# Performance work log

Hardware: AMD Instinct MI355X
Metric: run time of the kernel (lower is better)

## Reference

```python
import jax, jax.numpy as jnp
import numpy as np

B, Tu, Tm, Tz = 32, 128, 128, 32
V, H, E = 10000, 512, 128
S = E + H  # state_size


def setup_inputs() -> dict:
    key = jax.random.key(0)
    ks = jax.random.split(key, 24)
    u_input = jax.random.randint(ks[0], (B, Tu), 0, V)
    m_input = jax.random.randint(ks[1], (B, Tm), 0, V)
    pv_z_idx = jax.random.randint(ks[2], (B, Tz), 0, V)
    inp = {
        'u_input': u_input,
        'u_input_1hot': jax.nn.one_hot(u_input, V, dtype=jnp.float32),
        'u_hiddens': jax.random.normal(ks[3], (B, Tu, H), jnp.float32),
        'm_input': m_input,
        'm_input_1hot': jax.nn.one_hot(m_input, V, dtype=jnp.float32),
        'm_hiddens': jax.random.normal(ks[4], (B, Tm, H), jnp.float32),
        'pv_z_prob': jax.nn.softmax(jax.random.normal(ks[5], (B, Tz, V), jnp.float32), axis=-1),
        'pv_z_hidden': jax.random.normal(ks[6], (B, Tz, H), jnp.float32),
        'pv_z_idx': pv_z_idx,
        'emb_zt': jax.random.normal(ks[7], (B, 1, E), jnp.float32),
        'last_hidden': jax.random.normal(ks[8], (1, B, H), jnp.float32),
        # Attn params (concat attention: v . tanh(W [h; enc]))
        'W_attn': jax.random.normal(ks[9], (H, 2 * H), jnp.float32) * 0.02,
        'b_attn': jnp.zeros((H,), jnp.float32),
        'v_attn': jax.random.normal(ks[10], (H,), jnp.float32) * 0.05,
        # GRU params (torch gate order r,z,n)
        'W_ih': jax.random.normal(ks[11], (3 * H, S), jnp.float32) * 0.02,
        'W_hh': jax.random.normal(ks[12], (3 * H, H), jnp.float32) * 0.02,
        'b_ih': jnp.zeros((3 * H,), jnp.float32),
        'b_hh': jnp.zeros((3 * H,), jnp.float32),
        # generation / copy-score projections
        'W_gen': jax.random.normal(ks[13], (V, S), jnp.float32) * 0.02,
        'b_gen': jnp.zeros((V,), jnp.float32),
        'W_cpu': jax.random.normal(ks[14], (S, H), jnp.float32) * 0.02,
        'b_cpu': jnp.zeros((S,), jnp.float32),
        'W_cpm': jax.random.normal(ks[15], (S, H), jnp.float32) * 0.02,
        'b_cpm': jnp.zeros((S,), jnp.float32),
        'W_cppz': jax.random.normal(ks[16], (S, H), jnp.float32) * 0.02,
        'b_cppz': jnp.zeros((S,), jnp.float32),
    }
    return inp


def reference(u_input, u_input_1hot, u_hiddens, m_input, m_input_1hot, m_hiddens,
              pv_z_prob, pv_z_hidden, pv_z_idx, emb_zt, last_hidden,
              W_attn, b_attn, v_attn, W_ih, W_hh, b_ih, b_hh,
              W_gen, b_gen, W_cpu, b_cpu, W_cpm, b_cpm, W_cppz, b_cppz):
    Bv, Tuv, Vv = u_input_1hot.shape
    Tmv = m_hiddens.shape[1]
    t_input = emb_zt  # [B,1,E] (enable_selc_read=False)

    # ---- concat attention over [u; m; pv_z] hiddens ----
    enc = jnp.concatenate([u_hiddens, m_hiddens, pv_z_hidden], axis=1)  # [B,T,H]
    h0 = jnp.transpose(last_hidden, (1, 0, 2))  # [B,1,H]
    hid_rep = jnp.broadcast_to(h0, (Bv, enc.shape[1], h0.shape[2]))
    energy = jnp.tanh(jnp.einsum('bth,gh->btg', jnp.concatenate([hid_rep, enc], axis=2), W_attn) + b_attn)
    attn_w = jax.nn.softmax(jnp.einsum('bth,h->bt', energy, v_attn), axis=1)
    context = jnp.einsum('bt,bth->bh', attn_w, enc)[:, None, :]  # [B,1,H]

    # ---- single GRU step (torch gate order r,z,n) ----
    x = jnp.concatenate([t_input, context], axis=2)[:, 0, :]  # [B,E+H]
    h = h0[:, 0, :]
    gi = x @ W_ih.T + b_ih
    gh = h @ W_hh.T + b_hh
    i_r, i_z, i_n = jnp.split(gi, 3, axis=1)
    h_r, h_z, h_n = jnp.split(gh, 3, axis=1)
    r = jax.nn.sigmoid(i_r + h_r)
    z = jax.nn.sigmoid(i_z + h_z)
    n = jnp.tanh(i_n + r * h_n)
    h_new = (1.0 - z) * n + z * h  # [B,H]
    gru_out = h_new[:, None, :]
    last_hidden_new = h_new[None, :, :]

    # ---- generation + copy scores ----
    st = jnp.concatenate([h_new, t_input[:, 0, :]], axis=1)  # [B,E+H]
    score_g = st @ W_gen.T + b_gen  # [B,V]
    sc_u = jnp.einsum('bts,bs->bt', jnp.tanh(jnp.einsum('bth,sh->bts', u_hiddens, W_cpu) + b_cpu), st)
    sc_m = jnp.einsum('bts,bs->bt', jnp.tanh(jnp.einsum('bth,sh->bts', m_hiddens, W_cpm) + b_cpm), st)
    sc_pz = jnp.einsum('bts,bs->bt', jnp.tanh(jnp.einsum('bth,sh->bts', pv_z_hidden, W_cppz) + b_cppz), st)
    probs = jax.nn.softmax(jnp.concatenate([score_g, sc_u, sc_m, sc_pz], axis=1), axis=1)

    p_g = probs[:, :Vv]
    p_u = probs[:, Vv:Vv + Tuv]
    p_m = probs[:, Vv + Tuv:Vv + Tuv + Tmv]
    p_pz = probs[:, Vv + Tuv + Tmv:]
    prob_out = (p_g
                + jnp.einsum('bt,btv->bv', p_u, u_input_1hot)
                + jnp.einsum('bt,btv->bv', p_m, m_input_1hot)
                + jnp.einsum('bt,btv->bv', p_pz, pv_z_prob))
    return (prob_out, last_hidden_new, gru_out)
```

## Files before the change

### kernel.cpp

```cpp
#include <hip/hip_runtime.h>
#include <math.h>

#define B   32
#define TU  128
#define TM  128
#define TZ  32
#define TENC 288
#define V   10000
#define H   512
#define E   128
#define S   640
#define G3  1536
#define NLOG (V + TENC)

#define WS_Q      0
#define WS_SCORE  (WS_Q + B*H)
#define WS_CTX    (WS_SCORE + B*TENC)
#define WS_GI     (WS_CTX + B*H)
#define WS_GH     (WS_GI + B*G3)
#define WS_ST     (WS_GH + B*G3)
#define WS_LOGIT  (WS_ST + B*S)
#define WS_PCOPY  (WS_LOGIT + B*NLOG)
#define WS_F_TOTAL (WS_PCOPY + B*TENC)

#define BF_WA2  0
#define BF_WCP  (BF_WA2 + 512*512)
#define BF_ENC  (BF_WCP + 3*640*512)
#define BF_ST   (BF_ENC + B*TENC*H)
#define BF_TANH (BF_ST + B*S)

typedef __attribute__((ext_vector_type(8))) short bf16x8_t;
typedef __attribute__((ext_vector_type(4))) float f32x4_t;
typedef __attribute__((ext_vector_type(16))) float f32x16_t;

__device__ __forceinline__ float fast_tanh(float x) {
    return 1.f - 2.f / (__expf(2.f * x) + 1.f);
}

__device__ __forceinline__ unsigned short f2bf(float x) {
    unsigned int u = __float_as_uint(x);
    u += 0x7fffu + ((u >> 16) & 1u);
    return (unsigned short)(u >> 16);
}

__device__ __forceinline__ float bf2f(unsigned short u) {
    return __uint_as_float(((unsigned int)u) << 16);
}

__device__ __forceinline__ bf16x8_t cvt8(const float* p) {
    float4 a = *(const float4*)(p);
    float4 b = *(const float4*)(p + 4);
    bf16x8_t r;
    r[0] = (short)f2bf(a.x); r[1] = (short)f2bf(a.y);
    r[2] = (short)f2bf(a.z); r[3] = (short)f2bf(a.w);
    r[4] = (short)f2bf(b.x); r[5] = (short)f2bf(b.y);
    r[6] = (short)f2bf(b.z); r[7] = (short)f2bf(b.w);
    return r;
}

__device__ __forceinline__ const float* enc_row(const float* u, const float* m,
                                                const float* pz, int b, int t) {
    if (t < TU) return u + ((size_t)b * TU + t) * H;
    if (t < TU + TM) return m + ((size_t)b * TM + (t - TU)) * H;
    return pz + ((size_t)b * TZ + (t - TU - TM)) * H;
}

#define CVT_WA2_END  65536
#define CVT_TOTAL    (CVT_WA2_END + 3*81920)
#define CVTE_TOTAL   (B * TENC * 128)
#define CVT_ALL      (CVT_TOTAL + CVTE_TOTAL)
__global__ __launch_bounds__(256) void k_cvt_all(const float* __restrict__ W_attn,
                                                 const float* __restrict__ W_cpu,
                                                 const float* __restrict__ W_cpm,
                                                 const float* __restrict__ W_cppz,
                                                 const float* __restrict__ u_h,
                                                 const float* __restrict__ m_h,
                                                 const float* __restrict__ pz_h,
                                                 unsigned short* __restrict__ bf) {
    int idx = blockIdx.x * 256 + threadIdx.x;
    if (idx >= CVT_ALL) return;
    const float* src;
    unsigned short* dst;
    if (idx < CVT_WA2_END) {
        int g = idx >> 7, c4 = idx & 127;
        int k = c4 * 4, kt = k >> 5, kin = k & 31;
        src = W_attn + (size_t)g * 1024 + 512 + k;
        dst = bf + BF_WA2 + kt * (512 * 32) + g * 32 + kin;
    } else if (idx < CVT_TOTAL) {
        int r = idx - CVT_WA2_END;
        int seg = r / 81920, q = r % 81920;
        int s = q >> 7, c4 = q & 127;
        int k = c4 * 4, kt = k >> 5, kin = k & 31;
        const float* s0 = (seg == 0) ? W_cpu : (seg == 1) ? W_cpm : W_cppz;
        src = s0 + (size_t)s * 512 + k;
        dst = bf + BF_WCP + seg * 327680 + kt * (640 * 32) + s * 32 + kin;
    } else {
        int e = idx - CVT_TOTAL;
        int b = e / (TENC * 128);
        int r = e % (TENC * 128);
        int t = r >> 7, c4 = r & 127;
        int k = c4 * 4, kt = k >> 5, kin = k & 31;
        src = enc_row(u_h, m_h, pz_h, b, t) + k;
        dst = bf + BF_ENC + (((size_t)b * 16 + kt) * TENC + t) * 32 + kin;
    }
    float4 v = *(const float4*)src;
    ushort4 o;
    o.x = f2bf(v.x); o.y = f2bf(v.y); o.z = f2bf(v.z); o.w = f2bf(v.w);
    *(ushort4*)dst = o;
}

__global__ __launch_bounds__(64) void k_q_mfma(const float* __restrict__ last_h,
                                               const float* __restrict__ W_attn,
                                               const float* __restrict__ b_attn,
                                               float* __restrict__ ws) {
    int lane = threadIdx.x & 63;
    int m = lane & 31, khalf = lane >> 5;
    int n = blockIdx.x * 32 + m;
    const float* aptr = last_h + (size_t)m * H + khalf * 8;
    const float* bptr = W_attn + (size_t)n * 1024 + khalf * 8;
    f32x16_t acc = {};
    for (int k0 = 0; k0 < 512; k0 += 16) {
        bf16x8_t a = cvt8(aptr + k0);
        bf16x8_t bb = cvt8(bptr + k0);
        acc = __builtin_amdgcn_mfma_f32_32x32x16_bf16(a, bb, acc, 0, 0, 0);
    }
    float bg = b_attn[n];
#pragma unroll
    for (int r = 0; r < 16; ++r) {
        int row = (r & 3) + 8 * (r >> 2) + 4 * khalf;
        ws[WS_Q + row * H + n] = acc[r] + bg;
    }
}

__global__ __launch_bounds__(512) void k_enc_mfma(const unsigned short* __restrict__ bf,
                                                  const float* __restrict__ v_attn,
                                                  const float* __restrict__ b_cpu,
                                                  const float* __restrict__ b_cpm,
                                                  const float* __restrict__ b_cppz,
                                                  float* __restrict__ ws,
                                                  unsigned short* __restrict__ bft) {
    int blk = blockIdx.x;
    int b = blk / 9, t0 = (blk % 9) * 32;
    int tid = threadIdx.x, wave = tid >> 6, lane = tid & 63;
    int n16 = lane & 15, quad = lane >> 4;
    int seg = (t0 < TU) ? 0 : (t0 < TU + TM) ? 1 : 2;
    const float* bias = (seg == 0) ? b_cpu : (seg == 1) ? b_cpm : b_cppz;
    const unsigned short* abase =
        bf + BF_ENC + (((size_t)b * 16) * TENC + t0 + n16) * 32 + quad * 8;
    const unsigned short* wa =
        bf + BF_WA2 + (wave * 4) * (16 * 32) + n16 * 32 + quad * 8;
    const unsigned short* wc =
        bf + BF_WCP + seg * 327680 + (wave * 5) * (16 * 32) + n16 * 32 + quad * 8;
    f32x4_t accA[2][4], accC[2][5];
#pragma unroll
    for (int tl = 0; tl < 2; ++tl) {
#pragma unroll
        for (int j = 0; j < 4; ++j) accA[tl][j] = (f32x4_t){0.f, 0.f, 0.f, 0.f};
#pragma unroll
        for (int j = 0; j < 5; ++j) accC[tl][j] = (f32x4_t){0.f, 0.f, 0.f, 0.f};
    }
    for (int kt = 0; kt < 16; ++kt) {
        bf16x8_t a0 = *(const bf16x8_t*)(abase + (size_t)kt * TENC * 32);
        bf16x8_t a1 = *(const bf16x8_t*)(abase + (size_t)kt * TENC * 32 + 16 * 32);
        const unsigned short* wak = wa + (size_t)kt * 512 * 32;
        const unsigned short* wck = wc + (size_t)kt * 640 * 32;
#pragma unroll
        for (int j = 0; j < 4; ++j) {
            bf16x8_t bb = *(const bf16x8_t*)(wak + j * (16 * 32));
            accA[0][j] = __builtin_amdgcn_mfma_f32_16x16x32_bf16(a0, bb, accA[0][j], 0, 0, 0);
            accA[1][j] = __builtin_amdgcn_mfma_f32_16x16x32_bf16(a1, bb, accA[1][j], 0, 0, 0);
        }
#pragma unroll
        for (int j = 0; j < 5; ++j) {
            bf16x8_t bb = *(const bf16x8_t*)(wck + j * (16 * 32));
            accC[0][j] = __builtin_amdgcn_mfma_f32_16x16x32_bf16(a0, bb, accC[0][j], 0, 0, 0);
            accC[1][j] = __builtin_amdgcn_mfma_f32_16x16x32_bf16(a1, bb, accC[1][j], 0, 0, 0);
        }
    }
    float sval[2][4] = {{0.f, 0.f, 0.f, 0.f}, {0.f, 0.f, 0.f, 0.f}};
#pragma unroll
    for (int j = 0; j < 4; ++j) {
        int g = (wave * 4 + j) * 16 + n16;
        float q = ws[WS_Q + b * H + g];
        float va = v_attn[g];
#pragma unroll
        for (int tl = 0; tl < 2; ++tl)
#pragma unroll
            for (int r = 0; r < 4; ++r)
                sval[tl][r] += fast_tanh(accA[tl][j][r] + q) * va;
    }
#pragma unroll
    for (int tl = 0; tl < 2; ++tl)
#pragma unroll
        for (int r = 0; r < 4; ++r)
#pragma unroll
            for (int off = 8; off > 0; off >>= 1)
                sval[tl][r] += __shfl_down(sval[tl][r], off, 64);
    __shared__ float red[8][32];
    if (n16 == 0)
#pragma unroll
        for (int tl = 0; tl < 2; ++tl)
#pragma unroll
            for (int r = 0; r < 4; ++r)
                red[wave][tl * 16 + quad * 4 + r] = sval[tl][r];
#pragma unroll
    for (int j = 0; j < 5; ++j) {
        int s = (wave * 5 + j) * 16 + n16;
        float bi = bias[s];
#pragma unroll
        for (int tl = 0; tl < 2; ++tl)
#pragma unroll
            for (int r = 0; r < 4; ++r) {
                int t = t0 + tl * 16 + quad * 4 + r;
                bft[BF_TANH + ((size_t)b * TENC + t) * S + s] =
                    f2bf(fast_tanh(accC[tl][j][r] + bi));
            }
    }
    __syncthreads();
    if (tid < 32) {
        float v = 0.f;
#pragma unroll
        for (int w = 0; w < 8; ++w) v += red[w][tid];
        ws[WS_SCORE + b * TENC + t0 + tid] = v;
    }
}

__global__ __launch_bounds__(256) void k_softmax_ctx(const unsigned short* __restrict__ bf,
                                                     float* __restrict__ ws) {
    int b = blockIdx.x, tid = threadIdx.x;
    __shared__ float wsm[TENC];
    __shared__ float red1[4], red2[4];
    float local = -1e30f;
    for (int t = tid; t < TENC; t += 256) {
        float s = ws[WS_SCORE + b * TENC + t];
        wsm[t] = s;
        local = fmaxf(local, s);
    }
    int lane = tid & 63, wv = tid >> 6;
    for (int off = 32; off > 0; off >>= 1) local = fmaxf(local, __shfl_down(local, off, 64));
    if (lane == 0) red1[wv] = local;
    __syncthreads();
    float mx = fmaxf(fmaxf(red1[0], red1[1]), fmaxf(red1[2], red1[3]));
    float ls = 0.f;
    for (int t = tid; t < TENC; t += 256) {
        float e = __expf(wsm[t] - mx);
        wsm[t] = e;
        ls += e;
    }
    for (int off = 32; off > 0; off >>= 1) ls += __shfl_down(ls, off, 64);
    if (lane == 0) red2[wv] = ls;
    __syncthreads();
    float inv = 1.f / (red2[0] + red2[1] + red2[2] + red2[3]);

    int h2 = tid * 2;
    int kt = h2 >> 5, hin = h2 & 31;
    const unsigned short* ep = bf + BF_ENC + ((size_t)b * 16 + kt) * TENC * 32 + hin;
    float a00 = 0.f, a01 = 0.f, a10 = 0.f, a11 = 0.f;
#pragma unroll 2
    for (int t = 0; t < TENC; t += 2) {
        ushort2 v0 = *(const ushort2*)(ep + (size_t)t * 32);
        ushort2 v1 = *(const ushort2*)(ep + (size_t)(t + 1) * 32);
        float w0 = wsm[t], w1 = wsm[t + 1];
        a00 += w0 * bf2f(v0.x); a10 += w0 * bf2f(v0.y);
        a01 += w1 * bf2f(v1.x); a11 += w1 * bf2f(v1.y);
    }
    ws[WS_CTX + b * H + h2]     = (a00 + a01) * inv;
    ws[WS_CTX + b * H + h2 + 1] = (a10 + a11) * inv;
}

__global__ __launch_bounds__(64) void k_gru_mfma(const float* __restrict__ emb,
                                                 const float* __restrict__ last_h,
                                                 const float* __restrict__ W_ih,
                                                 const float* __restrict__ W_hh,
                                                 const float* __restrict__ b_ih,
                                                 const float* __restrict__ b_hh,
                                                 float* __restrict__ ws) {
    int blk = blockIdx.x;
    int lane = threadIdx.x & 63;
    int m = lane & 31, khalf = lane >> 5;
    if (blk < 48) {
        int n = blk * 32 + m;
        const float* bi_row = W_ih + (size_t)n * S + khalf * 8;
        f32x16_t acc = {};
        for (int k0 = 0; k0 < S; k0 += 16) {
            int ks = k0 + khalf * 8;
            const float* ap = (ks < E) ? (emb + m * E + ks)
                                       : (ws + WS_CTX + m * H + (ks - E));
            bf16x8_t a = cvt8(ap);
            bf16x8_t bb = cvt8(bi_row + k0);
            acc = __builtin_amdgcn_mfma_f32_32x32x16_bf16(a, bb, acc, 0, 0, 0);
        }
        float bi = b_ih[n];
#pragma unroll
        for (int r = 0; r < 16; ++r) {
            int row = (r & 3) + 8 * (r >> 2) + 4 * khalf;
            ws[WS_GI + row * G3 + n] = acc[r] + bi;
        }
    } else {
        int n = (blk - 48) * 32 + m;
        const float* bh_row = W_hh + (size_t)n * H + khalf * 8;
        const float* ah = last_h + (size_t)m * H + khalf * 8;
        f32x16_t acc = {};
        for (int k0 = 0; k0 < H; k0 += 16) {
            bf16x8_t a = cvt8(ah + k0);
            bf16x8_t bb = cvt8(bh_row + k0);
            acc = __builtin_amdgcn_mfma_f32_32x32x16_bf16(a, bb, acc, 0, 0, 0);
        }
        float bh = b_hh[n];
#pragma unroll
        for (int r = 0; r < 16; ++r) {
            int row = (r & 3) + 8 * (r >> 2) + 4 * khalf;
            ws[WS_GH + row * G3 + n] = acc[r] + bh;
        }
    }
}

__global__ __launch_bounds__(256) void k_fuse_copy(const float* __restrict__ emb,
                                                   const float* __restrict__ last_hidden,
                                                   const unsigned short* __restrict__ bft,
                                                   float* __restrict__ ws,
                                                   unsigned short* __restrict__ bf,
                                                   float* __restrict__ out) {
    int blk = blockIdx.x;
    int b = blk / 18, t0 = (blk % 18) * 16;
    int tid = threadIdx.x;
    __shared__ float st_s[S];
    for (int h = tid; h < H; h += 256) {
        float gi_r = ws[WS_GI + b * G3 + h];
        float gi_z = ws[WS_GI + b * G3 + H + h];
        float gi_n = ws[WS_GI + b * G3 + 2 * H + h];
        float gh_r = ws[WS_GH + b * G3 + h];
        float gh_z = ws[WS_GH + b * G3 + H + h];
        float gh_n = ws[WS_GH + b * G3 + 2 * H + h];
        float rr = 1.f / (1.f + __expf(-(gi_r + gh_r)));
        float zz = 1.f / (1.f + __expf(-(gi_z + gh_z)));
        float nn = fast_tanh(gi_n + rr * gh_n);
        float hp = last_hidden[b * H + h];
        float hn = (1.f - zz) * nn + zz * hp;
        st_s[h] = hn;
        if (t0 == 0) {
            out[V * B + b * H + h] = hn;
            out[V * B + B * H + b * H + h] = hn;
            bf[BF_ST + b * S + h] = f2bf(hn);
        }
    }
    if (tid < E) {
        float ev = emb[b * E + tid];
        st_s[H + tid] = ev;
        if (t0 == 0) bf[BF_ST + b * S + H + tid] = f2bf(ev);
    }
    __syncthreads();
    int wave = tid >> 6, lane = tid & 63;
#pragma unroll
    for (int tl = 0; tl < 4; ++tl) {
        int t = t0 + wave * 4 + tl;
        const unsigned short* row = bft + BF_TANH + ((size_t)b * TENC + t) * S;
        float acc = 0.f;
#pragma unroll
        for (int i = 0; i < 10; ++i) {
            int s = lane + 64 * i;
            acc += bf2f(row[s]) * st_s[s];
        }
        for (int off = 32; off > 0; off >>= 1) acc += __shfl_down(acc, off, 64);
        if (lane == 0) ws[WS_LOGIT + (size_t)b * NLOG + V + t] = acc;
    }
}

__global__ __launch_bounds__(64) void k_score_g_mfma(const unsigned short* __restrict__ bf,
                                                     const float* __restrict__ W_gen,
                                                     const float* __restrict__ b_gen,
                                                     float* __restrict__ ws) {
    int lane = threadIdx.x & 63;
    int m = lane & 31, khalf = lane >> 5;
    int n = blockIdx.x * 32 + m;
    int nr = (n < V) ? n : (V - 1);
    const unsigned short* aptr = bf + BF_ST + (size_t)m * S + khalf * 8;
    const float* bptr = W_gen + (size_t)nr * S + khalf * 8;
    f32x16_t acc = {};
    for (int k0 = 0; k0 < S; k0 += 16) {
        bf16x8_t a = *(const bf16x8_t*)(aptr + k0);
        bf16x8_t bb = cvt8(bptr + k0);
        acc = __builtin_amdgcn_mfma_f32_32x32x16_bf16(a, bb, acc, 0, 0, 0);
    }
    if (n >= V) return;
    float bg = b_gen[n];
#pragma unroll
    for (int r = 0; r < 16; ++r) {
        int row = (r & 3) + 8 * (r >> 2) + 4 * khalf;
        ws[WS_LOGIT + (size_t)row * NLOG + n] = acc[r] + bg;
    }
}

__global__ __launch_bounds__(512) void k_softmax_scatter(const int* __restrict__ u_in,
                                                         const int* __restrict__ m_in,
                                                         float* __restrict__ ws,
                                                         float* __restrict__ out) {
    int b = blockIdx.x, tid = threadIdx.x;
    __shared__ float red1[8], red2[8];
    __shared__ float ex[NLOG];
    const float* lg = ws + WS_LOGIT + (size_t)b * NLOG;
    float mx = -1e30f;
    for (int i = tid; i < NLOG; i += 512) {
        float v = lg[i];
        ex[i] = v;
        mx = fmaxf(mx, v);
    }
    int lane = tid & 63, wv = tid >> 6;
    for (int off = 32; off > 0; off >>= 1) mx = fmaxf(mx, __shfl_down(mx, off, 64));
    if (lane == 0) red1[wv] = mx;
    __syncthreads();
    mx = red1[0];
#pragma unroll
    for (int w = 1; w < 8; ++w) mx = fmaxf(mx, red1[w]);
    float sm = 0.f;
    for (int i = tid; i < NLOG; i += 512) {
        float e = __expf(ex[i] - mx);
        ex[i] = e;
        sm += e;
    }
    for (int off = 32; off > 0; off >>= 1) sm += __shfl_down(sm, off, 64);
    if (lane == 0) red2[wv] = sm;
    __syncthreads();
    sm = red2[0];
#pragma unroll
    for (int w = 1; w < 8; ++w) sm += red2[w];
    float inv = 1.f / sm;
    for (int i = tid; i < V; i += 512) out[b * V + i] = ex[i] * inv;
    __syncthreads();
    if (tid < TU + TM) {
        int idx = (tid < TU) ? u_in[b * TU + tid] : m_in[b * TM + (tid - TU)];
        atomicAdd(&out[(size_t)b * V + idx], ex[V + tid] * inv);
    } else if (tid < TENC) {
        ws[WS_PCOPY + b * TENC + tid] = ex[V + tid] * inv;
    }
}

__global__ __launch_bounds__(256) void k_pv(const float* __restrict__ pvp,
                                            const float* __restrict__ ws,
                                            float* __restrict__ out) {
    int b = blockIdx.y;
    int v = blockIdx.x * 256 + threadIdx.x;
    __shared__ float p[TZ];
    if (threadIdx.x < TZ) p[threadIdx.x] = ws[WS_PCOPY + b * TENC + TU + TM + threadIdx.x];
    __syncthreads();
    if (v >= V) return;
    float acc = 0.f;
#pragma unroll 4
    for (int t = 0; t < TZ; ++t) acc += p[t] * pvp[((size_t)b * TZ + t) * V + v];
    out[(size_t)b * V + v] += acc;
}

extern "C" void kernel_launch(void* const* d_in, const int* in_sizes, int n_in,
                              void* d_out, int out_size, void* d_ws, size_t ws_size,
                              hipStream_t stream) {
    const int*   u_input   = (const int*)d_in[0];
    const float* u_h       = (const float*)d_in[2];
    const int*   m_input   = (const int*)d_in[3];
    const float* m_h       = (const float*)d_in[5];
    const float* pv_prob   = (const float*)d_in[6];
    const float* pz_h      = (const float*)d_in[7];
    const float* emb       = (const float*)d_in[9];
    const float* last_h    = (const float*)d_in[10];
    const float* W_attn    = (const float*)d_in[11];
    const float* b_attn    = (const float*)d_in[12];
    const float* v_attn    = (const float*)d_in[13];
    const float* W_ih      = (const float*)d_in[14];
    const float* W_hh      = (const float*)d_in[15];
    const float* b_ih      = (const float*)d_in[16];
    const float* b_hh      = (const float*)d_in[17];
    const float* W_gen     = (const float*)d_in[18];
    const float* b_gen     = (const float*)d_in[19];
    const float* W_cpu     = (const float*)d_in[20];
    const float* b_cpu     = (const float*)d_in[21];
    const float* W_cpm     = (const float*)d_in[22];
    const float* b_cpm     = (const float*)d_in[23];
    const float* W_cppz    = (const float*)d_in[24];
    const float* b_cppz    = (const float*)d_in[25];
    float* ws  = (float*)d_ws;
    unsigned short* bf = (unsigned short*)(ws + WS_F_TOTAL);
    float* out = (float*)d_out;

    hipLaunchKernelGGL(k_cvt_all, dim3((CVT_ALL + 255) / 256), dim3(256), 0, stream,
                       W_attn, W_cpu, W_cpm, W_cppz, u_h, m_h, pz_h, bf);
    hipLaunchKernelGGL(k_q_mfma, dim3(16), dim3(64), 0, stream, last_h, W_attn, b_attn, ws);
    hipLaunchKernelGGL(k_enc_mfma, dim3(B * 9), dim3(512), 0, stream,
                       bf, v_attn, b_cpu, b_cpm, b_cppz, ws, bf);
    hipLaunchKernelGGL(k_softmax_ctx, dim3(B), dim3(256), 0, stream, bf, ws);
    hipLaunchKernelGGL(k_gru_mfma, dim3(96), dim3(64), 0, stream,
                       emb, last_h, W_ih, W_hh, b_ih, b_hh, ws);
    hipLaunchKernelGGL(k_fuse_copy, dim3(B * 18), dim3(256), 0, stream,
                       emb, last_h, bf, ws, bf, out);
    hipLaunchKernelGGL(k_score_g_mfma, dim3((V + 31) / 32), dim3(64), 0, stream,
                       bf, W_gen, b_gen, ws);
    hipLaunchKernelGGL(k_softmax_scatter, dim3(B), dim3(512), 0, stream,
                       u_input, m_input, ws, out);
    hipLaunchKernelGGL(k_pv, dim3(40, B), dim3(256), 0, stream, pv_prob, ws, out);
}
```

Baseline: 500.7 us.

## Restructure pipeline: hoist GRU matvecs into prep, split-K waves, split enc kernel

Moves the query projection, the W_hh matvec and the emb part of the W_ih matvec into the conversion kernel, so they run alongside the bf16 conversion before attention. Each matvec now splits K across four waves, with a shared-memory reduction, so blocks do more parallel work. The encoder kernel is split into separate attention-score and copy-tanh blocks with 256 threads each. The GRU gate combine is now its own small kernel, and the copy-score dot products are merged with the W_gen logits into one launch. The aim is more parallelism and less serial latency on the critical path, at the cost of extra shared-memory reductions and an additional read-modify-write of the GI buffer.

New measurement: 513.1 us. 1.02x slower.

```diff
diff --git a/kernel.cpp b/kernel.cpp
--- a/kernel.cpp
+++ b/kernel.cpp
@@ -69,15 +69,69 @@
 #define CVT_TOTAL    (CVT_WA2_END + 3*81920)
 #define CVTE_TOTAL   (B * TENC * 128)
 #define CVT_ALL      (CVT_TOTAL + CVTE_TOTAL)
-__global__ __launch_bounds__(256) void k_cvt_all(const float* __restrict__ W_attn,
-                                                 const float* __restrict__ W_cpu,
-                                                 const float* __restrict__ W_cpm,
-                                                 const float* __restrict__ W_cppz,
-                                                 const float* __restrict__ u_h,
-                                                 const float* __restrict__ m_h,
-                                                 const float* __restrict__ pz_h,
-                                                 unsigned short* __restrict__ bf) {
-    int idx = blockIdx.x * 256 + threadIdx.x;
+#define NMV          112
+__global__ __launch_bounds__(256) void k_prep(const float* __restrict__ W_attn,
+                                              const float* __restrict__ W_cpu,
+                                              const float* __restrict__ W_cpm,
+                                              const float* __restrict__ W_cppz,
+                                              const float* __restrict__ u_h,
+                                              const float* __restrict__ m_h,
+                                              const float* __restrict__ pz_h,
+                                              const float* __restrict__ last_h,
+                                              const float* __restrict__ emb,
+                                              const float* __restrict__ W_hh,
+                                              const float* __restrict__ W_ih,
+                                              const float* __restrict__ b_attn,
+                                              const float* __restrict__ b_hh,
+                                              const float* __restrict__ b_ih,
+                                              float* __restrict__ ws,
+                                              unsigned short* __restrict__ bf) {
+    int blk = blockIdx.x, tid = threadIdx.x;
+    __shared__ float redmv[4][64][16];
+    if (blk < NMV) {
+        int wave = tid >> 6, lane = tid & 63;
+        int m = lane & 31, khalf = lane >> 5;
+        f32x16_t acc = {};
+        int n;
+        if (blk < 16) {
+            n = blk * 32 + m;
+            const float* aptr = last_h + (size_t)m * H + khalf * 8;
+            const float* bptr = W_attn + (size_t)n * 1024 + khalf * 8;
+            for (int k0 = wave * 128; k0 < wave * 128 + 128; k0 += 16)
+                acc = __builtin_amdgcn_mfma_f32_32x32x16_bf16(cvt8(aptr + k0),
+                                                              cvt8(bptr + k0), acc, 0, 0, 0);
+        } else if (blk < 64) {
+            n = (blk - 16) * 32 + m;
+            const float* aptr = last_h + (size_t)m * H + khalf * 8;
+            const float* bptr = W_hh + (size_t)n * H + khalf * 8;
+            for (int k0 = wave * 128; k0 < wave * 128 + 128; k0 += 16)
+                acc = __builtin_amdgcn_mfma_f32_32x32x16_bf16(cvt8(aptr + k0),
+                                                              cvt8(bptr + k0), acc, 0, 0, 0);
+        } else {
+            n = (blk - 64) * 32 + m;
+            const float* aptr = emb + (size_t)m * E + khalf * 8;
+            const float* bptr = W_ih + (size_t)n * S + khalf * 8;
+            for (int k0 = wave * 32; k0 < wave * 32 + 32; k0 += 16)
+                acc = __builtin_amdgcn_mfma_f32_32x32x16_bf16(cvt8(aptr + k0),
+                                                              cvt8(bptr + k0), acc, 0, 0, 0);
+        }
+#pragma unroll
+        for (int r = 0; r < 16; ++r) redmv[wave][lane][r] = acc[r];
+        __syncthreads();
+        if (wave == 0) {
+#pragma unroll
+            for (int r = 0; r < 16; ++r) {
+                float v = redmv[0][lane][r] + redmv[1][lane][r] +
+                          redmv[2][lane][r] + redmv[3][lane][r];
+                int row = (r & 3) + 8 * (r >> 2) + 4 * khalf;
+                if (blk < 16)      ws[WS_Q  + row * H  + n] = v + b_attn[n];
+                else if (blk < 64) ws[WS_GH + row * G3 + n] = v + b_hh[n];
+                else               ws[WS_GI + row * G3 + n] = v + b_ih[n];
+            }
+        }
+        return;
+    }
+    int idx = (blk - NMV) * 256 + tid;
     if (idx >= CVT_ALL) return;
     const float* src;
     unsigned short* dst;
@@ -109,30 +163,7 @@
     *(ushort4*)dst = o;
 }
 
-__global__ __launch_bounds__(64) void k_q_mfma(const float* __restrict__ last_h,
-                                               const float* __restrict__ W_attn,
-                                               const float* __restrict__ b_attn,
-                                               float* __restrict__ ws) {
-    int lane = threadIdx.x & 63;
-    int m = lane & 31, khalf = lane >> 5;
-    int n = blockIdx.x * 32 + m;
-    const float* aptr = last_h + (size_t)m * H + khalf * 8;
-    const float* bptr = W_attn + (size_t)n * 1024 + khalf * 8;
-    f32x16_t acc = {};
-    for (int k0 = 0; k0 < 512; k0 += 16) {
-        bf16x8_t a = cvt8(aptr + k0);
-        bf16x8_t bb = cvt8(bptr + k0);
-        acc = __builtin_amdgcn_mfma_f32_32x32x16_bf16(a, bb, acc, 0, 0, 0);
-    }
-    float bg = b_attn[n];
-#pragma unroll
-    for (int r = 0; r < 16; ++r) {
-        int row = (r & 3) + 8 * (r >> 2) + 4 * khalf;
-        ws[WS_Q + row * H + n] = acc[r] + bg;
-    }
-}
-
-__global__ __launch_bounds__(512) void k_enc_mfma(const unsigned short* __restrict__ bf,
+__global__ __launch_bounds__(256) void k_enc_mfma(const unsigned short* __restrict__ bf,
                                                   const float* __restrict__ v_attn,
                                                   const float* __restrict__ b_cpu,
                                                   const float* __restrict__ b_cpm,
@@ -140,88 +171,96 @@
                                                   float* __restrict__ ws,
                                                   unsigned short* __restrict__ bft) {
     int blk = blockIdx.x;
-    int b = blk / 9, t0 = (blk % 9) * 32;
+    int typeC = blk & 1;
+    int idx = blk >> 1;
+    int b = idx / 9, t0 = (idx % 9) * 32;
     int tid = threadIdx.x, wave = tid >> 6, lane = tid & 63;
     int n16 = lane & 15, quad = lane >> 4;
-    int seg = (t0 < TU) ? 0 : (t0 < TU + TM) ? 1 : 2;
-    const float* bias = (seg == 0) ? b_cpu : (seg == 1) ? b_cpm : b_cppz;
     const unsigned short* abase =
         bf + BF_ENC + (((size_t)b * 16) * TENC + t0 + n16) * 32 + quad * 8;
-    const unsigned short* wa =
-        bf + BF_WA2 + (wave * 4) * (16 * 32) + n16 * 32 + quad * 8;
-    const unsigned short* wc =
-        bf + BF_WCP + seg * 327680 + (wave * 5) * (16 * 32) + n16 * 32 + quad * 8;
-    f32x4_t accA[2][4], accC[2][5];
-#pragma unroll
-    for (int tl = 0; tl < 2; ++tl) {
-#pragma unroll
-        for (int j = 0; j < 4; ++j) accA[tl][j] = (f32x4_t){0.f, 0.f, 0.f, 0.f};
-#pragma unroll
-        for (int j = 0; j < 5; ++j) accC[tl][j] = (f32x4_t){0.f, 0.f, 0.f, 0.f};
-    }
-    for (int kt = 0; kt < 16; ++kt) {
-        bf16x8_t a0 = *(const bf16x8_t*)(abase + (size_t)kt * TENC * 32);
-        bf16x8_t a1 = *(const bf16x8_t*)(abase + (size_t)kt * TENC * 32 + 16 * 32);
-        const unsigned short* wak = wa + (size_t)kt * 512 * 32;
-        const unsigned short* wck = wc + (size_t)kt * 640 * 32;
-#pragma unroll
-        for (int j = 0; j < 4; ++j) {
-            bf16x8_t bb = *(const bf16x8_t*)(wak + j * (16 * 32));
-            accA[0][j] = __builtin_amdgcn_mfma_f32_16x16x32_bf16(a0, bb, accA[0][j], 0, 0, 0);
-            accA[1][j] = __builtin_amdgcn_mfma_f32_16x16x32_bf16(a1, bb, accA[1][j], 0, 0, 0);
-        }
-#pragma unroll
-        for (int j = 0; j < 5; ++j) {
-            bf16x8_t bb = *(const bf16x8_t*)(wck + j * (16 * 32));
-            accC[0][j] = __builtin_amdgcn_mfma_f32_16x16x32_bf16(a0, bb, accC[0][j], 0, 0, 0);
-            accC[1][j] = __builtin_amdgcn_mfma_f32_16x16x32_bf16(a1, bb, accC[1][j], 0, 0, 0);
-        }
-    }
-    float sval[2][4] = {{0.f, 0.f, 0.f, 0.f}, {0.f, 0.f, 0.f, 0.f}};
-#pragma unroll
-    for (int j = 0; j < 4; ++j) {
-        int g = (wave * 4 + j) * 16 + n16;
-        float q = ws[WS_Q + b * H + g];
-        float va = v_attn[g];
+    if (!typeC) {
+        const unsigned short* wa =
+            bf + BF_WA2 + (wave * 8) * (16 * 32) + n16 * 32 + quad * 8;
+        f32x4_t acc[2][8];
 #pragma unroll
         for (int tl = 0; tl < 2; ++tl)
 #pragma unroll
+            for (int j = 0; j < 8; ++j) acc[tl][j] = (f32x4_t){0.f, 0.f, 0.f, 0.f};
+        for (int kt = 0; kt < 16; ++kt) {
+            bf16x8_t a0 = *(const bf16x8_t*)(abase + (size_t)kt * TENC * 32);
+            bf16x8_t a1 = *(const bf16x8_t*)(abase + (size_t)kt * TENC * 32 + 16 * 32);
+            const unsigned short* wak = wa + (size_t)kt * 512 * 32;
+#pragma unroll
+            for (int j = 0; j < 8; ++j) {
+                bf16x8_t bb = *(const bf16x8_t*)(wak + j * (16 * 32));
+                acc[0][j] = __builtin_amdgcn_mfma_f32_16x16x32_bf16(a0, bb, acc[0][j], 0, 0, 0);
+                acc[1][j] = __builtin_amdgcn_mfma_f32_16x16x32_bf16(a1, bb, acc[1][j], 0, 0, 0);
+            }
+        }
+        float sval[2][4] = {{0.f, 0.f, 0.f, 0.f}, {0.f, 0.f, 0.f, 0.f}};
+#pragma unroll
+        for (int j = 0; j < 8; ++j) {
+            int g = (wave * 8 + j) * 16 + n16;
+            float q = ws[WS_Q + b * H + g];
+            float va = v_attn[g];
+#pragma unroll
+            for (int tl = 0; tl < 2; ++tl)
+#pragma unroll
+                for (int r = 0; r < 4; ++r)
+                    sval[tl][r] += fast_tanh(acc[tl][j][r] + q) * va;
+        }
+#pragma unroll
+        for (int tl = 0; tl < 2; ++tl)
+#pragma unroll
             for (int r = 0; r < 4; ++r)
-                sval[tl][r] += fast_tanh(accA[tl][j][r] + q) * va;
-    }
-#pragma unroll
-    for (int tl = 0; tl < 2; ++tl)
-#pragma unroll
-        for (int r = 0; r < 4; ++r)
-#pragma unroll
-            for (int off = 8; off > 0; off >>= 1)
-                sval[tl][r] += __shfl_down(sval[tl][r], off, 64);
-    __shared__ float red[8][32];
-    if (n16 == 0)
+#pragma unroll
+                for (int off = 8; off > 0; off >>= 1)
+                    sval[tl][r] += __shfl_down(sval[tl][r], off, 64);
+        __shared__ float red[4][32];
+        if (n16 == 0)
+#pragma unroll
+            for (int tl = 0; tl < 2; ++tl)
+#pragma unroll
+                for (int r = 0; r < 4; ++r)
+                    red[wave][tl * 16 + quad * 4 + r] = sval[tl][r];
+        __syncthreads();
+        if (tid < 32)
+            ws[WS_SCORE + b * TENC + t0 + tid] =
+                red[0][tid] + red[1][tid] + red[2][tid] + red[3][tid];
+    } else {
+        int seg = (t0 < TU) ? 0 : (t0 < TU + TM) ? 1 : 2;
+        const float* bias = (seg == 0) ? b_cpu : (seg == 1) ? b_cpm : b_cppz;
+        const unsigned short* wc =
+            bf + BF_WCP + seg * 327680 + (wave * 10) * (16 * 32) + n16 * 32 + quad * 8;
+        f32x4_t acc[2][10];
 #pragma unroll
         for (int tl = 0; tl < 2; ++tl)
 #pragma unroll
-            for (int r = 0; r < 4; ++r)
-                red[wave][tl * 16 + quad * 4 + r] = sval[tl][r];
-#pragma unroll
-    for (int j = 0; j < 5; ++j) {
-        int s = (wave * 5 + j) * 16 + n16;
-        float bi = bias[s];
-#pragma unroll
-        for (int tl = 0; tl < 2; ++tl)
-#pragma unroll
-            for (int r = 0; r < 4; ++r) {
-                int t = t0 + tl * 16 + quad * 4 + r;
-                bft[BF_TANH + ((size_t)b * TENC + t) * S + s] =
-                    f2bf(fast_tanh(accC[tl][j][r] + bi));
+            for (int j = 0; j < 10; ++j) acc[tl][j] = (f32x4_t){0.f, 0.f, 0.f, 0.f};
+        for (int kt = 0; kt < 16; ++kt) {
+            bf16x8_t a0 = *(const bf16x8_t*)(abase + (size_t)kt * TENC * 32);
+            bf16x8_t a1 = *(const bf16x8_t*)(abase + (size_t)kt * TENC * 32 + 16 * 32);
+            const unsigned short* wck = wc + (size_t)kt * 640 * 32;
+#pragma unroll
+            for (int j = 0; j < 10; ++j) {
+                bf16x8_t bb = *(const bf16x8_t*)(wck + j * (16 * 32));
+                acc[0][j] = __builtin_amdgcn_mfma_f32_16x16x32_bf16(a0, bb, acc[0][j], 0, 0, 0);
+                acc[1][j] = __builtin_amdgcn_mfma_f32_16x16x32_bf16(a1, bb, acc[1][j], 0, 0, 0);
             }
-    }
-    __syncthreads();
-    if (tid < 32) {
-        float v = 0.f;
-#pragma unroll
-        for (int w = 0; w < 8; ++w) v += red[w][tid];
-        ws[WS_SCORE + b * TENC + t0 + tid] = v;
+        }
+#pragma unroll
+        for (int j = 0; j < 10; ++j) {
+            int s = (wave * 10 + j) * 16 + n16;
+            float bi = bias[s];
+#pragma unroll
+            for (int tl = 0; tl < 2; ++tl)
+#pragma unroll
+                for (int r = 0; r < 4; ++r) {
+                    int t = t0 + tl * 16 + quad * 4 + r;
+                    bft[BF_TANH + ((size_t)b * TENC + t) * S + s] =
+                        f2bf(fast_tanh(acc[tl][j][r] + bi));
+                }
+        }
     }
 }
 
@@ -268,126 +307,111 @@
     ws[WS_CTX + b * H + h2 + 1] = (a10 + a11) * inv;
 }
 
-__global__ __launch_bounds__(64) void k_gru_mfma(const float* __restrict__ emb,
-                                                 const float* __restrict__ last_h,
-                                                 const float* __restrict__ W_ih,
-                                                 const float* __restrict__ W_hh,
-                                                 const float* __restrict__ b_ih,
-                                                 const float* __restrict__ b_hh,
+__global__ __launch_bounds__(256) void k_gru_ctx(const float* __restrict__ W_ih,
                                                  float* __restrict__ ws) {
-    int blk = blockIdx.x;
-    int lane = threadIdx.x & 63;
+    int blk = blockIdx.x, tid = threadIdx.x;
+    __shared__ float redmv[4][64][16];
+    int wave = tid >> 6, lane = tid & 63;
     int m = lane & 31, khalf = lane >> 5;
-    if (blk < 48) {
-        int n = blk * 32 + m;
-        const float* bi_row = W_ih + (size_t)n * S + khalf * 8;
+    int n = blk * 32 + m;
+    const float* aptr = ws + WS_CTX + (size_t)m * H + khalf * 8;
+    const float* bptr = W_ih + (size_t)n * S + E + khalf * 8;
+    f32x16_t acc = {};
+    for (int k0 = wave * 128; k0 < wave * 128 + 128; k0 += 16)
+        acc = __builtin_amdgcn_mfma_f32_32x32x16_bf16(cvt8(aptr + k0),
+                                                      cvt8(bptr + k0), acc, 0, 0, 0);
+#pragma unroll
+    for (int r = 0; r < 16; ++r) redmv[wave][lane][r] = acc[r];
+    __syncthreads();
+    if (wave == 0) {
+#pragma unroll
+        for (int r = 0; r < 16; ++r) {
+            float v = redmv[0][lane][r] + redmv[1][lane][r] +
+                      redmv[2][lane][r] + redmv[3][lane][r];
+            int row = (r & 3) + 8 * (r >> 2) + 4 * khalf;
+            ws[WS_GI + row * G3 + n] += v;
+        }
+    }
+}
+
+__global__ __launch_bounds__(256) void k_combine(const float* __restrict__ emb,
+                                                 const float* __restrict__ last_hidden,
+                                                 float* __restrict__ ws,
+                                                 unsigned short* __restrict__ bf,
+                                                 float* __restrict__ out) {
+    int i = blockIdx.x * 256 + threadIdx.x;
+    int b = i >> 9, h = i & 511;
+    float gi_r = ws[WS_GI + b * G3 + h];
+    float gi_z = ws[WS_GI + b * G3 + H + h];
+    float gi_n = ws[WS_GI + b * G3 + 2 * H + h];
+    float gh_r = ws[WS_GH + b * G3 + h];
+    float gh_z = ws[WS_GH + b * G3 + H + h];
+    float gh_n = ws[WS_GH + b * G3 + 2 * H + h];
+    float rr = 1.f / (1.f + __expf(-(gi_r + gh_r)));
+    float zz = 1.f / (1.f + __expf(-(gi_z + gh_z)));
+    float nn = fast_tanh(gi_n + rr * gh_n);
+    float hp = last_hidden[b * H + h];
+    float hn = (1.f - zz) * nn + zz * hp;
+    out[V * B + b * H + h] = hn;
+    out[V * B + B * H + b * H + h] = hn;
+    ws[WS_ST + b * S + h] = hn;
+    bf[BF_ST + b * S + h] = f2bf(hn);
+    if (h < E) {
+        float ev = emb[b * E + h];
+        ws[WS_ST + b * S + H + h] = ev;
+        bf[BF_ST + b * S + H + h] = f2bf(ev);
+    }
+}
+
+__global__ __launch_bounds__(256) void k_logits(const unsigned short* __restrict__ bf,
+                                                const float* __restrict__ W_gen,
+                                                const float* __restrict__ b_gen,
+                                                float* __restrict__ ws) {
+    int blk = blockIdx.x, tid = threadIdx.x;
+    __shared__ float shmem[4 * 64 * 16];
+    int wave = tid >> 6, lane = tid & 63;
+    if (blk < 576) {
+        int b = blk / 18, t0 = (blk % 18) * 16;
+        float* st_s = shmem;
+        for (int i = tid; i < S; i += 256) st_s[i] = ws[WS_ST + b * S + i];
+        __syncthreads();
+#pragma unroll
+        for (int tl = 0; tl < 4; ++tl) {
+            int t = t0 + wave * 4 + tl;
+            const unsigned short* row = bf + BF_TANH + ((size_t)b * TENC + t) * S;
+            float acc = 0.f;
+#pragma unroll
+            for (int i = 0; i < 10; ++i) {
+                int s = lane + 64 * i;
+                acc += bf2f(row[s]) * st_s[s];
+            }
+            for (int off = 32; off > 0; off >>= 1) acc += __shfl_down(acc, off, 64);
+            if (lane == 0) ws[WS_LOGIT + (size_t)b * NLOG + V + t] = acc;
+        }
+    } else {
+        float (*redmv)[64][16] = (float (*)[64][16])shmem;
+        int m = lane & 31, khalf = lane >> 5;
+        int n = (blk - 576) * 32 + m;
+        int nr = (n < V) ? n : (V - 1);
+        const unsigned short* aptr = bf + BF_ST + (size_t)m * S + khalf * 8;
+        const float* bptr = W_gen + (size_t)nr * S + khalf * 8;
         f32x16_t acc = {};
-        for (int k0 = 0; k0 < S; k0 += 16) {
-            int ks = k0 + khalf * 8;
-            const float* ap = (ks < E) ? (emb + m * E + ks)
-                                       : (ws + WS_CTX + m * H + (ks - E));
-            bf16x8_t a = cvt8(ap);
-            bf16x8_t bb = cvt8(bi_row + k0);
-            acc = __builtin_amdgcn_mfma_f32_32x32x16_bf16(a, bb, acc, 0, 0, 0);
-        }
-        float bi = b_ih[n];
-#pragma unroll
-        for (int r = 0; r < 16; ++r) {
-            int row = (r & 3) + 8 * (r >> 2) + 4 * khalf;
-            ws[WS_GI + row * G3 + n] = acc[r] + bi;
-        }
-    } else {
-        int n = (blk - 48) * 32 + m;
-        const float* bh_row = W_hh + (size_t)n * H + khalf * 8;
-        const float* ah = last_h + (size_t)m * H + khalf * 8;
-        f32x16_t acc = {};
-        for (int k0 = 0; k0 < H; k0 += 16) {
-            bf16x8_t a = cvt8(ah + k0);
-            bf16x8_t bb = cvt8(bh_row + k0);
-            acc = __builtin_amdgcn_mfma_f32_32x32x16_bf16(a, bb, acc, 0, 0, 0);
-        }
-        float bh = b_hh[n];
-#pragma unroll
-        for (int r = 0; r < 16; ++r) {
-            int row = (r & 3) + 8 * (r >> 2) + 4 * khalf;
-            ws[WS_GH + row * G3 + n] = acc[r] + bh;
-        }
-    }
-}
-
-__global__ __launch_bounds__(256) void k_fuse_copy(const float* __restrict__ emb,
-                                                   const float* __restrict__ last_hidden,
-                                                   const unsigned short* __restrict__ bft,
-                                                   float* __restrict__ ws,
-                                                   unsigned short* __restrict__ bf,
-                                                   float* __restrict__ out) {
-    int blk = blockIdx.x;
-    int b = blk / 18, t0 = (blk % 18) * 16;
-    int tid = threadIdx.x;
-    __shared__ float st_s[S];
-    for (int h = tid; h < H; h += 256) {
-        float gi_r = ws[WS_GI + b * G3 + h];
-        float gi_z = ws[WS_GI + b * G3 + H + h];
-        float gi_n = ws[WS_GI + b * G3 + 2 * H + h];
-        float gh_r = ws[WS_GH + b * G3 + h];
-        float gh_z = ws[WS_GH + b * G3 + H + h];
-        float gh_n = ws[WS_GH + b * G3 + 2 * H + h];
-        float rr = 1.f / (1.f + __expf(-(gi_r + gh_r)));
-        float zz = 1.f / (1.f + __expf(-(gi_z + gh_z)));
-        float nn = fast_tanh(gi_n + rr * gh_n);
-        float hp = last_hidden[b * H + h];
-        float hn = (1.f - zz) * nn + zz * hp;
-        st_s[h] = hn;
-        if (t0 == 0) {
-            out[V * B + b * H + h] = hn;
-            out[V * B + B * H + b * H + h] = hn;
-            bf[BF_ST + b * S + h] = f2bf(hn);
-        }
-    }
-    if (tid < E) {
-        float ev = emb[b * E + tid];
-        st_s[H + tid] = ev;
-        if (t0 == 0) bf[BF_ST + b * S + H + tid] = f2bf(ev);
-    }
-    __syncthreads();
-    int wave = tid >> 6, lane = tid & 63;
-#pragma unroll
-    for (int tl = 0; tl < 4; ++tl) {
-        int t = t0 + wave * 4 + tl;
-        const unsigned short* row = bft + BF_TANH + ((size_t)b * TENC + t) * S;
-        float acc = 0.f;
-#pragma unroll
-        for (int i = 0; i < 10; ++i) {
-            int s = lane + 64 * i;
-            acc += bf2f(row[s]) * st_s[s];
-        }
-        for (int off = 32; off > 0; off >>= 1) acc += __shfl_down(acc, off, 64);
-        if (lane == 0) ws[WS_LOGIT + (size_t)b * NLOG + V + t] = acc;
-    }
-}
-
-__global__ __launch_bounds__(64) void k_score_g_mfma(const unsigned short* __restrict__ bf,
-                                                     const float* __restrict__ W_gen,
-                                                     const float* __restrict__ b_gen,
-                                                     float* __restrict__ ws) {
-    int lane = threadIdx.x & 63;
-    int m = lane & 31, khalf = lane >> 5;
-    int n = blockIdx.x * 32 + m;
-    int nr = (n < V) ? n : (V - 1);
-    const unsigned short* aptr = bf + BF_ST + (size_t)m * S + khalf * 8;
-    const float* bptr = W_gen + (size_t)nr * S + khalf * 8;
-    f32x16_t acc = {};
-    for (int k0 = 0; k0 < S; k0 += 16) {
-        bf16x8_t a = *(const bf16x8_t*)(aptr + k0);
-        bf16x8_t bb = cvt8(bptr + k0);
-        acc = __builtin_amdgcn_mfma_f32_32x32x16_bf16(a, bb, acc, 0, 0, 0);
-    }
-    if (n >= V) return;
-    float bg = b_gen[n];
-#pragma unroll
-    for (int r = 0; r < 16; ++r) {
-        int row = (r & 3) + 8 * (r >> 2) + 4 * khalf;
-        ws[WS_LOGIT + (size_t)row * NLOG + n] = acc[r] + bg;
+        for (int k0 = wave * 160; k0 < wave * 160 + 160; k0 += 16)
+            acc = __builtin_amdgcn_mfma_f32_32x32x16_bf16(*(const bf16x8_t*)(aptr + k0),
+                                                          cvt8(bptr + k0), acc, 0, 0, 0);
+#pragma unroll
+        for (int r = 0; r < 16; ++r) redmv[wave][lane][r] = acc[r];
+        __syncthreads();
+        if (wave == 0 && n < V) {
+            float bg = b_gen[n];
+#pragma unroll
+            for (int r = 0; r < 16; ++r) {
+                float v = redmv[0][lane][r] + redmv[1][lane][r] +
+                          redmv[2][lane][r] + redmv[3][lane][r];
+                int row = (r & 3) + 8 * (r >> 2) + 4 * khalf;
+                ws[WS_LOGIT + (size_t)row * NLOG + n] = v + bg;
+            }
+        }
     }
 }
 
@@ -480,18 +504,15 @@
     unsigned short* bf = (unsigned short*)(ws + WS_F_TOTAL);
     float* out = (float*)d_out;
 
-    hipLaunchKernelGGL(k_cvt_all, dim3((CVT_ALL + 255) / 256), dim3(256), 0, stream,
-                       W_attn, W_cpu, W_cpm, W_cppz, u_h, m_h, pz_h, bf);
-    hipLaunchKernelGGL(k_q_mfma, dim3(16), dim3(64), 0, stream, last_h, W_attn, b_attn, ws);
-    hipLaunchKernelGGL(k_enc_mfma, dim3(B * 9), dim3(512), 0, stream,
+    hipLaunchKernelGGL(k_prep, dim3(NMV + CVT_ALL / 256), dim3(256), 0, stream,
+                       W_attn, W_cpu, W_cpm, W_cppz, u_h, m_h, pz_h,
+                       last_h, emb, W_hh, W_ih, b_attn, b_hh, b_ih, ws, bf);
+    hipLaunchKernelGGL(k_enc_mfma, dim3(576), dim3(256), 0, stream,
                        bf, v_attn, b_cpu, b_cpm, b_cppz, ws, bf);
     hipLaunchKernelGGL(k_softmax_ctx, dim3(B), dim3(256), 0, stream, bf, ws);
-    hipLaunchKernelGGL(k_gru_mfma, dim3(96), dim3(64), 0, stream,
-                       emb, last_h, W_ih, W_hh, b_ih, b_hh, ws);
-    hipLaunchKernelGGL(k_fuse_copy, dim3(B * 18), dim3(256), 0, stream,
-                       emb, last_h, bf, ws, bf, out);
-    hipLaunchKernelGGL(k_score_g_mfma, dim3((V + 31) / 32), dim3(64), 0, stream,
-                       bf, W_gen, b_gen, ws);
+    hipLaunchKernelGGL(k_gru_ctx, dim3(48), dim3(256), 0, stream, W_ih, ws);
+    hipLaunchKernelGGL(k_combine, dim3(64), dim3(256), 0, stream, emb, last_h, ws, bf, out);
+    hipLaunchKernelGGL(k_logits, dim3(576 + 313), dim3(256), 0, stream, bf, W_gen, b_gen, ws);
     hipLaunchKernelGGL(k_softmax_scatter, dim3(B), dim3(512), 0, stream,
                        u_input, m_input, ws, out);
     hipLaunchKernelGGL(k_pv, dim3(40, B), dim3(256), 0, stream, pv_prob, ws, out);
```
